# Kernel tuning notes

Hardware: AMD Instinct MI355X
Metric: run time of the kernel (lower is better)

## Reference

```python
import jax, jax.numpy as jnp
import numpy as np

IN_CH, OUT_CH, M1, M2 = 64, 64, 32, 32


def _powerlaw_psd_gaussian(key, exponent, n):
    """JAX port of colorednoise.powerlaw_psd_gaussian (fmin=0 default)."""
    f = jnp.fft.rfftfreq(n).astype(jnp.float32)  # [n//2+1]
    # fmin = max(0, 1/n); f[0]=0 is the only freq below it -> clamp to f[1]
    s_scale = jnp.where(f < 1.0 / n, f[1], f) ** (-exponent / 2.0)
    w = s_scale[1:]
    w = w.at[-1].multiply((1 + (n % 2)) / 2.0)  # Nyquist correction
    sigma = 2.0 * jnp.sqrt(jnp.sum(w * w)) / n
    kr, ki = jax.random.split(key)
    sr = jax.random.normal(kr, f.shape, jnp.float32) * s_scale
    si = jax.random.normal(ki, f.shape, jnp.float32) * s_scale
    if n % 2 == 0:
        si = si.at[-1].set(0.0)
        sr = sr.at[-1].multiply(jnp.sqrt(2.0))
    si = si.at[0].set(0.0)
    sr = sr.at[0].multiply(jnp.sqrt(2.0))
    return jnp.fft.irfft(sr + 1j * si, n=n) / sigma


def _compl_mul2d(t1, w, e_r, e_i, amp_r, amp_i, phi_r, phi_i, key):
    # Faithful to the torch code: stack over in-ch at dim=1 then sum dim=2
    # sums over the OUT channel axis => out[b,i,x,y] = t1[b,i,x,y]*sum_o w[i,o,x,y]
    out = t1 * jnp.sum(w, axis=1)[None]  # [B, IN_CH, M1, M2] complex
    b, c, m1, m2 = out.shape
    n = b * c * m1 * m2
    k1, k2 = jax.random.split(key)
    nr = jnp.roll(_powerlaw_psd_gaussian(k1, e_r, n), phi_r.astype(jnp.int32)) * amp_r
    ni = jnp.roll(_powerlaw_psd_gaussian(k2, e_i, n), phi_i.astype(jnp.int32)) * amp_i
    # original multiplies imag noise by amp_i twice (once in-place, once on reshape)
    noise = (nr + 1j * (ni * amp_i)).reshape(b, c, m1, m2)
    return out - noise


def _forward(x, w1, w2, exp_r, exp_i, nAmp_real, nAmp_imag, nPhase_real, nphase_imag):
    w1c = w1[..., 0] + 1j * w1[..., 1]  # [IN, OUT, M1, M2] complex64
    w2c = w2[..., 0] + 1j * w2[..., 1]
    e_r = jnp.median(exp_r)
    e_i = jnp.median(exp_i)
    amp_r = jnp.median(nAmp_real)
    amp_i = jnp.median(nAmp_imag)
    phi_r = jnp.median(nPhase_real)
    phi_i = jnp.median(nphase_imag)
    B, _, H, W = x.shape
    Wr = W // 2 + 1
    x_ft = jnp.fft.rfft2(x)  # [B, IN_CH, H, Wr]
    key = jax.random.key(42)
    kA, kB = jax.random.split(key)
    out_ft = jnp.zeros((B, OUT_CH, H, Wr), jnp.complex64)
    out_ft = out_ft.at[:, :, :M1, :M2].set(
        _compl_mul2d(x_ft[:, :, :M1, :M2], w1c, e_r, e_i, amp_r, amp_i, phi_r, phi_i, kA))
    out_ft = out_ft.at[:, :, -M1:, :M2].set(
        _compl_mul2d(x_ft[:, :, -M1:, :M2], w2c, e_r, e_i, amp_r, amp_i, phi_r, phi_i, kB))
    return jnp.fft.irfft2(out_ft, s=(H, W)).astype(jnp.float32)


def setup_inputs() -> dict:
    key = jax.random.key(0)
    ks = jax.random.split(key, 9)
    scale = 1.0 / (IN_CH * OUT_CH)
    return {
        "x": jax.random.normal(ks[0], (16, IN_CH, 256, 256), jnp.float32),
        "w1": scale * jax.random.uniform(ks[1], (IN_CH, OUT_CH, M1, M2, 2), jnp.float32),
        "w2": scale * jax.random.uniform(ks[2], (IN_CH, OUT_CH, M1, M2, 2), jnp.float32),
        "exp_r": jax.random.uniform(ks[3], (8,), jnp.float32),
        "exp_i": jax.random.uniform(ks[4], (8,), jnp.float32),
        "nAmp_real": jax.random.uniform(ks[5], (8,), jnp.float32),
        "nAmp_imag": jax.random.uniform(ks[6], (8,), jnp.float32),
        "nPhase_real": jax.random.normal(ks[7], (8,), jnp.float32),
        "nphase_imag": jax.random.normal(ks[8], (8,), jnp.float32),
    }


def reference(x, w1, w2, exp_r, exp_i, nAmp_real, nAmp_imag, nPhase_real, nphase_imag):
    return _forward(x, w1, w2, exp_r, exp_i, nAmp_real, nAmp_imag, nPhase_real, nphase_imag)
```

## Files before the change

kernel.cpp:

```cpp
#include <hip/hip_runtime.h>
#include <cstdint>

#define JPART 1
#define PART_XOR 1

constexpr uint32_t N20   = 1u << 20;
constexpr uint32_t NHALF = 1u << 19;
constexpr int SPT_STRIDE = 520;

struct Hdr {
  float e_r, e_i, amp_r, amp_i;
  int   phi_r, phi_i;
  float nhe_r, nhe_i;
  float scale_s[4];
};
struct KeyArgs { uint32_t k[8][2]; };

typedef __attribute__((ext_vector_type(8))) short short8;
typedef __attribute__((ext_vector_type(16))) float f32x16;

__device__ inline f32x16 zero16() {
  f32x16 v;
  #pragma unroll
  for (int i = 0; i < 16; ++i) v[i] = 0.f;
  return v;
}

__device__ inline unsigned short f2bf(float f) {
  uint32_t u = __float_as_uint(f);
  return (unsigned short)((u + 0x7fffu + ((u >> 16) & 1u)) >> 16);
}

__host__ __device__ inline void tf2x32(uint32_t k0, uint32_t k1, uint32_t x0, uint32_t x1,
                                       uint32_t& o0, uint32_t& o1) {
  const uint32_t ks0 = k0, ks1 = k1, ks2 = k0 ^ k1 ^ 0x1BD11BDAu;
  const uint32_t ks[3] = { ks0, ks1, ks2 };
  x0 += ks0; x1 += ks1;
  const int rot[2][4] = { {13,15,26,6}, {17,29,16,24} };
  for (int g = 0; g < 5; ++g) {
    const int* rr = rot[g & 1];
    for (int i = 0; i < 4; ++i) {
      x0 += x1;
      x1 = (x1 << rr[i]) | (x1 >> (32 - rr[i]));
      x1 ^= x0;
    }
    x0 += ks[(g + 1) % 3];
    x1 += ks[(g + 2) % 3] + (uint32_t)(g + 1);
  }
  o0 = x0; o1 = x1;
}

__device__ inline float erfinv_xla(float x) {
  float w = -log1pf(-x * x);
  float p;
  if (w < 5.0f) {
    w -= 2.5f;
    p = 2.81022636e-08f;
    p = fmaf(p, w, 3.43273939e-07f);
    p = fmaf(p, w, -3.5233877e-06f);
    p = fmaf(p, w, -4.39150654e-06f);
    p = fmaf(p, w, 0.00021858087f);
    p = fmaf(p, w, -0.00125372503f);
    p = fmaf(p, w, -0.00417768164f);
    p = fmaf(p, w, 0.246640727f);
    p = fmaf(p, w, 1.50140941f);
  } else {
    w = sqrtf(w) - 3.0f;
    p = -0.000200214257f;
    p = fmaf(p, w, 0.000100950558f);
    p = fmaf(p, w, 0.00134934322f);
    p = fmaf(p, w, -0.00367342844f);
    p = fmaf(p, w, 0.00573950773f);
    p = fmaf(p, w, -0.0076224613f);
    p = fmaf(p, w, 0.00943887047f);
    p = fmaf(p, w, 1.00167406f);
    p = fmaf(p, w, 2.83297682f);
  }
  return p * x;
}

__device__ inline float normal_from_bits(uint32_t bits) {
  uint32_t fb = (bits >> 9) | 0x3f800000u;
  float f = __uint_as_float(fb) - 1.0f;
  const float LO = -0.99999994f;
  float u = f * 2.0f + LO;
  u = fmaxf(LO, u);
  return 1.41421356f * erfinv_xla(u);
}

__device__ inline float sscale_f(uint32_t k, float nhe) {
  uint32_t kk = k ? k : 1u;
  return powf((float)kk * (1.0f / 1048576.0f), nhe);
}

__device__ inline float2 cmul(float2 a, float2 b) {
  return make_float2(a.x * b.x - a.y * b.y, a.x * b.y + a.y * b.x);
}
__device__ inline float2 wexp(float u) {
  float s, c; sincospif(2.0f * u, &s, &c); return make_float2(c, s);
}
__device__ inline float2 cadd(float2 a, float2 b){ return make_float2(a.x+b.x, a.y+b.y); }
__device__ inline float2 csub(float2 a, float2 b){ return make_float2(a.x-b.x, a.y-b.y); }
__device__ inline float2 cmuli(float2 a){ return make_float2(-a.y, a.x); }

__device__ inline int sA(int p) { return p ^ (((p >> 6) & 3) << 2) ^ ((p >> 8) & 3); }

__device__ inline void bfly(float2& y0, float2& y1, float2& y2, float2& y3, float2 W) {
  float2 a = cadd(y0, y2), b = csub(y0, y2);
  float2 c = cadd(y1, y3), d = cmuli(csub(y1, y3));
  float2 W2 = cmul(W, W), W3 = cmul(W2, W);
  y0 = cadd(a, c);
  y1 = cmul(cadd(b, d), W);
  y2 = cmul(csub(a, c), W2);
  y3 = cmul(csub(b, d), W3);
}

__device__ inline void fft1024_core(float2* r, float2* rc, float2* buf, int w) {
  #pragma unroll
  for (int e3 = 0; e3 < 4; ++e3) {
    float2 W = wexp((float)((e3 << 6) + w) * (1.0f / 1024.0f));
    bfly(r[e3], r[e3 + 4], r[e3 + 8], r[e3 + 12], W);
  }
  {
    float2 W = wexp((float)w * (1.0f / 256.0f));
    #pragma unroll
    for (int e4 = 0; e4 < 4; ++e4)
      bfly(r[(e4 << 2) + 0], r[(e4 << 2) + 1], r[(e4 << 2) + 2], r[(e4 << 2) + 3], W);
  }
  #pragma unroll
  for (int s = 0; s < 16; ++s) buf[sA((s << 6) + w)] = r[s];
  __syncthreads();
  {
    const int e0 = w & 3;
    const int pbase = ((w >> 4) << 8) + (((w >> 2) & 3) << 6) + e0;
    float2 rb[16];
    #pragma unroll
    for (int e2 = 0; e2 < 4; ++e2)
      #pragma unroll
      for (int e1 = 0; e1 < 4; ++e1)
        rb[(e2 << 2) + e1] = buf[sA(pbase + (e2 << 4) + (e1 << 2))];
    #pragma unroll
    for (int e1 = 0; e1 < 4; ++e1) {
      float2 W = wexp((float)((e1 << 2) + e0) * (1.0f / 64.0f));
      bfly(rb[e1], rb[e1 + 4], rb[e1 + 8], rb[e1 + 12], W);
    }
    {
      float2 W = wexp((float)e0 * (1.0f / 16.0f));
      #pragma unroll
      for (int e2 = 0; e2 < 4; ++e2)
        bfly(rb[(e2 << 2) + 0], rb[(e2 << 2) + 1], rb[(e2 << 2) + 2], rb[(e2 << 2) + 3], W);
    }
    #pragma unroll
    for (int e2 = 0; e2 < 4; ++e2)
      #pragma unroll
      for (int e1 = 0; e1 < 4; ++e1)
        buf[sA(pbase + (e2 << 4) + (e1 << 2))] = rb[(e2 << 2) + e1];
  }
  __syncthreads();
  {
    const int cbase = ((w >> 4) << 8) + (((w >> 2) & 3) << 6) + ((w & 3) << 4);
    #pragma unroll
    for (int e1 = 0; e1 < 4; ++e1)
      #pragma unroll
      for (int e0 = 0; e0 < 4; ++e0)
        rc[(e1 << 2) + e0] = buf[sA(cbase + (e1 << 2) + e0)];
    #pragma unroll
    for (int e1 = 0; e1 < 4; ++e1) {
      float2 x0 = rc[(e1 << 2)], x1 = rc[(e1 << 2) + 1], x2 = rc[(e1 << 2) + 2], x3 = rc[(e1 << 2) + 3];
      float2 a = cadd(x0, x2), b = csub(x0, x2);
      float2 c = cadd(x1, x3), d = cmuli(csub(x1, x3));
      rc[(e1 << 2)]     = cadd(a, c);
      rc[(e1 << 2) + 1] = cadd(b, d);
      rc[(e1 << 2) + 2] = csub(a, c);
      rc[(e1 << 2) + 3] = csub(b, d);
    }
  }
}

__device__ inline float med8_dev(const float* p) {
  float v[8];
  for (int i = 0; i < 8; ++i) v[i] = p[i];
  for (int i = 1; i < 8; ++i) { float key = v[i]; int j = i - 1;
    while (j >= 0 && v[j] > key) { v[j + 1] = v[j]; --j; } v[j + 1] = key; }
  return 0.5f * (v[3] + v[4]);
}

__global__ __launch_bounds__(256) void k_misc(Hdr* h,
    const float* er, const float* ei, const float* ar, const float* ai,
    const float* pr, const float* pim,
    const float* __restrict__ w1, const float* __restrict__ w2,
    float2* __restrict__ wsum,
    unsigned short* __restrict__ A_E, unsigned short* __restrict__ B2T,
    unsigned short* __restrict__ ET, unsigned short* __restrict__ Fc,
    unsigned short* __restrict__ Fs, unsigned short* __restrict__ Fns) {
  const int b = blockIdx.x;
  if (b == 960) {
    if (threadIdx.x) return;
    float mer = med8_dev(er), mei = med8_dev(ei);
    h->e_r = mer; h->e_i = mei;
    h->amp_r = med8_dev(ar); h->amp_i = med8_dev(ai);
    h->phi_r = (int)med8_dev(pr);
    h->phi_i = (int)med8_dev(pim);
    h->nhe_r = -0.5f * mer; h->nhe_i = -0.5f * mei;
    return;
  }
  if (b < 512) {
    int idx = b * 256 + threadIdx.x;
    int sel = idx >> 16, rem = idx & 65535;
    const float* w = sel ? w2 : w1;
    int c = rem >> 10, m1 = (rem >> 5) & 31, m2 = rem & 31;
    size_t base = (size_t)c * 131072 + (size_t)m1 * 64 + (size_t)m2 * 2;
    float sr = 0.f, si = 0.f;
    for (int oc = 0; oc < 64; ++oc) { sr += w[base + (size_t)oc * 2048]; si += w[base + (size_t)oc * 2048 + 1]; }
    wsum[idx] = make_float2(sr, si);
    return;
  }
  int t = (b - 512) * 256 + threadIdx.x;
  if (t < 32768) {
    int y = t >> 7, p = t & 127;
    int kyp = p & 63; int ky = (kyp < 32) ? kyp : kyp + 192;
    float s, c; sincospif(2.0f * (float)((ky * y) & 255) * (1.0f / 256.0f), &s, &c);
    A_E[t] = f2bf((p < 64) ? c : s);
  } else if (t < 49152) {
    int u = t - 32768;
    int x = u >> 6, j = u & 63, kx = j & 31;
    float s, c; sincospif(2.0f * (float)((kx * x) & 255) * (1.0f / 256.0f), &s, &c);
    float v = (j < 32) ? ((kx == 0) ? 1.0f : 2.0f * c)
                       : ((kx == 0) ? 0.0f : -2.0f * s);
    B2T[u] = f2bf(v * (1.0f / 65536.0f));
  } else if (t < 65536) {
    int u = t - 49152;
    int col = u >> 8, xx = u & 255; int kx = col & 31;
    float s, c; sincospif(2.0f * (float)((kx * xx) & 255) * (1.0f / 256.0f), &s, &c);
    ET[u] = f2bf((col < 32) ? c : -s);
  } else if (t < 114688) {
    int u = (t - 65536) & 16383;
    int which = (t - 65536) >> 14;
    int kyp = u >> 8, y = u & 255; int ky = (kyp < 32) ? kyp : kyp + 192;
    float s, c; sincospif(2.0f * (float)((ky * y) & 255) * (1.0f / 256.0f), &s, &c);
    if (which == 0) Fc[u] = f2bf(c);
    else if (which == 1) Fs[u] = f2bf(s);
    else Fns[u] = f2bf(-s);
  }
}

__global__ __launch_bounds__(256) void k_gen(const Hdr* __restrict__ h,
                                             float* __restrict__ partials,
                                             float4* __restrict__ spT, KeyArgs ka) {
  __shared__ float sr_[256], si_[256];
  const int b = blockIdx.x;
  if (b < 512) {
    const float nher = h->nhe_r, nhei = h->nhe_i;
    float sr = 0.f, si = 0.f;
    for (int j = 0; j < 4; ++j) {
      uint32_t k = (uint32_t)(b * 1024 + j * 256 + threadIdx.x) + 1u;
      float fk = (float)k * (1.0f / 1048576.0f);
      float wr = powf(fk, nher), wi = powf(fk, nhei);
      if (k == NHALF) { wr *= 0.5f; wi *= 0.5f; }
      sr += wr * wr; si += wi * wi;
    }
    sr_[threadIdx.x] = sr; si_[threadIdx.x] = si; __syncthreads();
    for (int off = 128; off > 0; off >>= 1) {
      if ((int)threadIdx.x < off) { sr_[threadIdx.x] += sr_[threadIdx.x + off];
                                    si_[threadIdx.x] += si_[threadIdx.x + off]; }
      __syncthreads();
    }
    if (!threadIdx.x) { partials[b * 2] = sr_[0]; partials[b * 2 + 1] = si_[0]; }
    return;
  }
  const int idx = b - 512;
  const int pair = idx >> 11;
  const int bx = idx & 2047;
  const int k1 = bx >> 1, chunk = bx & 1;
  const int k2 = (chunk << 8) + (int)threadIdx.x;
  const float nher = h->nhe_r, nhei = h->nhe_i;
  float4* row = spT + (size_t)pair * (1024 * SPT_STRIDE) + (size_t)k1 * SPT_STRIDE;
  const bool extra = (k1 == 0) && (chunk == 1) && (threadIdx.x == 255);
  const int niter = extra ? 2 : 1;
  for (int it = 0; it < niter; ++it) {
    const int kk2 = (it == 0) ? k2 : 512;
    const uint32_t i = (uint32_t)k1 + ((uint32_t)kk2 << 10);
    float vals[4];
    #pragma unroll
    for (int j = 0; j < 4; ++j) {
      const uint32_t K0 = ka.k[pair * 4 + j][0], K1 = ka.k[pair * 4 + j][1];
      uint32_t o0, o1; tf2x32(K0, K1, 0u, i, o0, o1);
#if PART_XOR
      uint32_t bits = o0 ^ o1;
#else
      uint32_t bits = o1;
#endif
      float nhe = (j < 2) ? nher : nhei;
      float v = normal_from_bits(bits) * sscale_f(i, nhe);
      if (i == 0u || i == NHALF) v = (j & 1) ? 0.0f : v * 1.41421356f;
      vals[j] = v;
    }
    row[kk2] = make_float4(vals[0], vals[1], vals[2], vals[3]);
  }
}

__global__ void k_sumw2_fin(Hdr* h, const float* partials) {
  if (threadIdx.x || blockIdx.x) return;
  float Sr = 0.f, Si = 0.f;
  for (int b = 0; b < 512; ++b) { Sr += partials[b * 2]; Si += partials[b * 2 + 1]; }
  float sig_r = 2.0f * sqrtf(Sr) * (1.0f / 1048576.0f);
  float sig_i = 2.0f * sqrtf(Si) * (1.0f / 1048576.0f);
  float s0 = h->amp_r / (sig_r * 1048576.0f);
  float s1 = (h->amp_i * h->amp_i) / (sig_i * 1048576.0f);
  h->scale_s[0] = s0; h->scale_s[1] = s1; h->scale_s[2] = s0; h->scale_s[3] = s1;
}

__global__ __launch_bounds__(256) void k_fft_s1(const float4* __restrict__ spT,
                                                float2* __restrict__ G) {
  __shared__ float2 buf4[4][1024];
  const int b = blockIdx.x;
  const int lin = (b & 7) * 64 + (b >> 3);
  const int pair = lin >> 8;
  const int g = threadIdx.x >> 6, w = threadIdx.x & 63;
  const int k1b = (lin & 255) << 2;
  const int k1 = k1b + g;
  const float4* sp = spT + (size_t)pair * (1024 * SPT_STRIDE);
  const int mrow = (1024 - k1) & 1023;

  float2 r[16], rc[16];
  #pragma unroll
  for (int s = 0; s < 16; ++s) {
    int k2 = (s << 6) + w;
    uint32_t k = (uint32_t)k1 + ((uint32_t)k2 << 10);
    float4 f; float2 z;
    if (k <= NHALF) {
      f = sp[(size_t)k1 * SPT_STRIDE + k2];
      z = make_float2(f.x - f.w, f.y + f.z);
    } else {
      int k2p = (k1 == 0) ? (1024 - k2) : (1023 - k2);
      f = sp[(size_t)mrow * SPT_STRIDE + k2p];
      z = make_float2(f.x + f.w, f.z - f.y);
    }
    r[s] = z;
  }
  fft1024_core(r, rc, buf4[g], w);
  const int klo = ((w & 3) << 4) + (((w >> 2) & 3) << 2) + (w >> 4);
  #pragma unroll
  for (int e1 = 0; e1 < 4; ++e1)
    #pragma unroll
    for (int e0 = 0; e0 < 4; ++e0) {
      int k = (e0 << 8) + (e1 << 6) + klo;
      float2 tw = wexp((float)(k * k1) * (1.0f / 1048576.0f));
      buf4[g][sA(k)] = cmul(rc[(e1 << 2) + e0], tw);
    }
  __syncthreads();
  const int t = threadIdx.x;
  float2* gp = G + ((size_t)pair << 20) + (size_t)k1b;
  const int k1off = t & 3;
  #pragma unroll
  for (int it = 0; it < 16; ++it) {
    int j2 = (it << 6) + (t >> 2);
    gp[((size_t)j2 << 10) + k1off] = buf4[k1off][sA(j2)];
  }
}

__global__ __launch_bounds__(256) void k_fft_s2(const float2* __restrict__ G,
                                                float2* __restrict__ noiseP,
                                                const Hdr* __restrict__ h) {
  __shared__ float2 buf4[4][1024];
  const int b = blockIdx.x;
  const int lin = (b & 7) * 64 + (b >> 3);
  const int pair = lin >> 8;
  const int g = threadIdx.x >> 6, w = threadIdx.x & 63;
  const int j2 = ((lin & 255) << 2) + g;

  float2 r[16], rc[16];
  const float2* gp = G + ((size_t)pair << 20) + ((size_t)j2 << 10);
  #pragma unroll
  for (int s = 0; s < 16; ++s) r[s] = gp[(s << 6) + w];
  fft1024_core(r, rc, buf4[g], w);
  const float scr = h->scale_s[0], sci = h->scale_s[1];
  float2* np_ = noiseP + ((size_t)pair << 20) + ((size_t)j2 << 10);
  const int klo = ((w & 3) << 4) + (((w >> 2) & 3) << 2) + (w >> 4);
  #pragma unroll
  for (int e1 = 0; e1 < 4; ++e1)
    #pragma unroll
    for (int e0 = 0; e0 < 4; ++e0) {
      int k = (e0 << 8) + (e1 << 6) + klo;
      np_[k] = make_float2(rc[(e1 << 2) + e0].x * scr, rc[(e1 << 2) + e0].y * sci);
    }
}

__global__ __launch_bounds__(256) void k_ntrans(const float2* __restrict__ noiseP,
                                                float* __restrict__ noiseL,
                                                const Hdr* __restrict__ h) {
  __shared__ float tr[64][65];
  __shared__ float ti[64][65];
  const int b = blockIdx.x;
  const int pair = b >> 8, tid = b & 255;
  const int R0 = (tid >> 4) << 6;
  const int C0 = (tid & 15) << 6;
  const int t = threadIdx.x;
  const int tx = t & 63, ty = t >> 6;
  const int phir = h->phi_r, phii = h->phi_i;
  const float2* src = noiseP + ((size_t)pair << 20);
  float* dstr = noiseL + ((size_t)(pair * 2) << 20);
  float* dsti = noiseL + ((size_t)(pair * 2 + 1) << 20);
  #pragma unroll
  for (int i = 0; i < 16; ++i) {
    int r = (i << 2) + ty;
    float2 v = src[(size_t)((R0 + r) << 10) + (size_t)(C0 + tx)];
    tr[r][tx] = v.x; ti[r][tx] = v.y;
  }
  __syncthreads();
  #pragma unroll
  for (int i = 0; i < 16; ++i) {
    int c = (i << 2) + ty;
    int n = ((C0 + c) << 10) + R0 + tx;
    dstr[(uint32_t)(n + phir) & (N20 - 1u)] = tr[tx][c];
    dsti[(uint32_t)(n + phii) & (N20 - 1u)] = ti[tx][c];
  }
}

__global__ __launch_bounds__(256, 2) void k_forward(const float* __restrict__ x,
    const float2* __restrict__ wsum, const float* __restrict__ noiseL,
    const unsigned short* __restrict__ ET, const unsigned short* __restrict__ Fc,
    const unsigned short* __restrict__ Fs, const unsigned short* __restrict__ Fns,
    float2* __restrict__ oftg) {
  __shared__ char lds[65536];
  char* X1T = lds + 32768;
  const int bc = blockIdx.x, t = threadIdx.x;
  const int c = bc & 63;
  const int l = t & 63, w = t >> 6, lr = l & 31, kg = l >> 5;
  const int rt = w >> 1, ct = w & 1;
  const float* xim = x + ((size_t)bc << 16);

  float4 pf[16];
  #pragma unroll
  for (int i = 0; i < 16; ++i) {
    int f4 = i * 256 + t;
    int r = f4 >> 6, c4 = f4 & 63;
    pf[i] = *(const float4*)(xim + (size_t)((r) << 8) + (c4 << 2));
  }

  #pragma unroll
  for (int yt = 0; yt < 4; ++yt) {
    __syncthreads();
    #pragma unroll
    for (int i = 0; i < 16; ++i) {
      int f4 = i * 256 + t;
      int r = f4 >> 6, c4 = f4 & 63;
      ushort4 b4; b4.x = f2bf(pf[i].x); b4.y = f2bf(pf[i].y);
      b4.z = f2bf(pf[i].z); b4.w = f2bf(pf[i].w);
      int byte = ((r << 9) + (c4 << 3)) ^ ((r & 7) << 4);
      *(ushort4*)(lds + byte) = b4;
    }
    __syncthreads();
    if (yt < 3) {
      #pragma unroll
      for (int i = 0; i < 16; ++i) {
        int f4 = i * 256 + t;
        int r = f4 >> 6, c4 = f4 & 63;
        pf[i] = *(const float4*)(xim + (size_t)((((yt + 1) << 6) + r) << 8) + (c4 << 2));
      }
    }
    f32x16 a1 = zero16();
    const int arow = (rt << 5) + lr;
    const int bcol = (ct << 5) + lr;
    #pragma unroll
    for (int s = 0; s < 16; ++s) {
      short8 af = *(const short8*)(lds + (((arow << 9) + (s << 5) + (kg << 4)) ^ ((arow & 7) << 4)));
      short8 bf = *(const short8*)(ET + (bcol << 8) + (s << 4) + (kg << 3));
      a1 = __builtin_amdgcn_mfma_f32_32x32x16_bf16(af, bf, a1, 0, 0, 0);
    }
    #pragma unroll
    for (int r4 = 0; r4 < 4; ++r4) {
      int y0 = (yt << 6) + (rt << 5) + (r4 << 3) + (kg << 2);
      ushort4 p4;
      p4.x = f2bf(a1[r4 * 4 + 0]); p4.y = f2bf(a1[r4 * 4 + 1]);
      p4.z = f2bf(a1[r4 * 4 + 2]); p4.w = f2bf(a1[r4 * 4 + 3]);
      int byte = ((bcol << 9) + (y0 << 1)) ^ ((bcol & 7) << 4);
      *(ushort4*)(X1T + byte) = p4;
    }
  }
  __syncthreads();

  const int re_im = w >> 1, kt = w & 1;
  const unsigned short* A1p = re_im ? Fns : Fs;
  const int b0row = (re_im ? 32 : 0) + lr;
  const int b1row = (re_im ? 0 : 32) + lr;
  const int a2row = (kt << 5) + lr;
  f32x16 a2 = zero16();
  #pragma unroll
  for (int s = 0; s < 16; ++s) {
    short8 a0f = *(const short8*)(Fc  + (a2row << 8) + (s << 4) + (kg << 3));
    short8 a1f = *(const short8*)(A1p + (a2row << 8) + (s << 4) + (kg << 3));
    short8 b0f = *(const short8*)(X1T + (((b0row << 9) + (s << 5) + (kg << 4)) ^ ((b0row & 7) << 4)));
    short8 b1f = *(const short8*)(X1T + (((b1row << 9) + (s << 5) + (kg << 4)) ^ ((b1row & 7) << 4)));
    a2 = __builtin_amdgcn_mfma_f32_32x32x16_bf16(a0f, b0f, a2, 0, 0, 0);
    a2 = __builtin_amdgcn_mfma_f32_32x32x16_bf16(a1f, b1f, a2, 0, 0, 0);
  }
  float* Osm = (float*)(lds + (re_im << 13));
  #pragma unroll
  for (int i = 0; i < 16; ++i) {
    int row = (kt << 5) + (i & 3) + ((i >> 2) << 3) + (kg << 2);
    Osm[(row << 5) + lr] = a2[i];
  }
  __syncthreads();

  const float* Ore = (const float*)lds;
  const float* Oim = (const float*)(lds + 8192);
  #pragma unroll
  for (int r = 0; r < 8; ++r) {
    int idx = (r << 8) + t;
    int kyp = idx >> 5, kx = idx & 31;
    int sel = kyp >> 5, m1 = kyp & 31;
    float2 av = make_float2(Ore[idx], Oim[idx]);
    float2 wv = wsum[((size_t)sel << 16) + (size_t)(((c << 5) | m1) << 5) + (size_t)kx];
    float2 v;
    v.x = av.x * wv.x - av.y * wv.y;
    v.y = av.x * wv.y + av.y * wv.x;
    uint32_t p = ((uint32_t)((bc << 5) | m1) << 5) | (uint32_t)kx;
    const float* nlr = noiseL + ((size_t)(sel ? 2 : 0) << 20);
    const float* nli = noiseL + ((size_t)(sel ? 3 : 1) << 20);
    v.x -= nlr[p];
    v.y -= nli[p];
    oftg[((size_t)bc << 11) + (size_t)idx] = v;
  }
}

__global__ __launch_bounds__(256) void k_inverse(const float2* __restrict__ oftg,
    const unsigned short* __restrict__ A_E, const unsigned short* __restrict__ B2T,
    float* __restrict__ out) {
  __shared__ char smem[32768];

  const int bc = blockIdx.x, t = threadIdx.x;
  const int l = t & 63, w = t >> 6, lr = l & 31, kg = l >> 5;

  {
    const float* ob = (const float*)(oftg + ((size_t)bc << 11));
    #pragma unroll
    for (int i = 0; i < 32; ++i) {
      int idx = t + (i << 8);
      int p = idx >> 6, j = idx & 63;
      int kyp = p & 63;
      float v;
      if (p < 64) v = (j < 32) ? ob[(kyp << 6) + (j << 1)]
                               : ob[(kyp << 6) + ((j - 32) << 1) + 1];
      else        v = (j < 32) ? -ob[(kyp << 6) + (j << 1) + 1]
                               : ob[(kyp << 6) + ((j - 32) << 1)];
      int byte = ((j << 8) + (p << 1)) ^ ((j & 7) << 4);
      *(unsigned short*)(smem + byte) = f2bf(v);
    }
  }
  __syncthreads();

  f32x16 acc[2][2];
  acc[0][0] = zero16(); acc[0][1] = zero16(); acc[1][0] = zero16(); acc[1][1] = zero16();
  #pragma unroll
  for (int s = 0; s < 8; ++s) {
    short8 af[2], bf[2];
    #pragma unroll
    for (int rt = 0; rt < 2; ++rt) {
      int row = (w << 6) + (rt << 5) + lr;
      af[rt] = *(const short8*)(A_E + (row << 7) + (s << 4) + (kg << 3));
    }
    #pragma unroll
    for (int ct = 0; ct < 2; ++ct) {
      int j = (ct << 5) + lr;
      int byte = ((j << 8) + (s << 5) + (kg << 4)) ^ ((j & 7) << 4);
      bf[ct] = *(const short8*)(smem + byte);
    }
    #pragma unroll
    for (int rt = 0; rt < 2; ++rt)
      #pragma unroll
      for (int ct = 0; ct < 2; ++ct)
        acc[rt][ct] = __builtin_amdgcn_mfma_f32_32x32x16_bf16(af[rt], bf[ct], acc[rt][ct], 0, 0, 0);
  }
  __syncthreads();

  #pragma unroll
  for (int rt = 0; rt < 2; ++rt)
    #pragma unroll
    for (int ct = 0; ct < 2; ++ct)
      #pragma unroll
      for (int r = 0; r < 16; ++r) {
        int row = (w << 6) + (rt << 5) + (r & 3) + (((r >> 2) & 3) << 3) + (kg << 2);
        int col = (ct << 5) + lr;
        int byte = ((row << 7) + (col << 1)) ^ ((row & 7) << 4);
        *(unsigned short*)(smem + byte) = f2bf(acc[rt][ct][r]);
      }
  __syncthreads();

  short8 ta[2][4];
  #pragma unroll
  for (int rt = 0; rt < 2; ++rt)
    #pragma unroll
    for (int ks = 0; ks < 4; ++ks) {
      int row = (w << 6) + (rt << 5) + lr;
      int byte = ((row << 7) + (ks << 5) + (kg << 4)) ^ ((row & 7) << 4);
      ta[rt][ks] = *(const short8*)(smem + byte);
    }
  float* op = out + ((size_t)bc << 16);
  #pragma unroll
  for (int cc = 0; cc < 4; ++cc) {
    short8 b2[2][4];
    #pragma unroll
    for (int cx = 0; cx < 2; ++cx)
      #pragma unroll
      for (int ks = 0; ks < 4; ++ks) {
        int xx = (cc << 6) + (cx << 5) + lr;
        b2[cx][ks] = *(const short8*)(B2T + (xx << 6) + (ks << 4) + (kg << 3));
      }
    f32x16 a2[2][2];
    a2[0][0] = zero16(); a2[0][1] = zero16(); a2[1][0] = zero16(); a2[1][1] = zero16();
    #pragma unroll
    for (int ks = 0; ks < 4; ++ks)
      #pragma unroll
      for (int rt = 0; rt < 2; ++rt)
        #pragma unroll
        for (int cx = 0; cx < 2; ++cx)
          a2[rt][cx] = __builtin_amdgcn_mfma_f32_32x32x16_bf16(ta[rt][ks], b2[cx][ks], a2[rt][cx], 0, 0, 0);
    #pragma unroll
    for (int rt = 0; rt < 2; ++rt)
      #pragma unroll
      for (int cx = 0; cx < 2; ++cx)
        #pragma unroll
        for (int r = 0; r < 16; ++r) {
          int row = (w << 6) + (rt << 5) + (r & 3) + (((r >> 2) & 3) << 3) + (kg << 2);
          int xx = (cc << 6) + (cx << 5) + lr;
          op[(row << 8) + xx] = a2[rt][cx][r];
        }
  }
}

extern "C" void kernel_launch(void* const* d_in, const int* in_sizes, int n_in,
                              void* d_out, int out_size, void* d_ws, size_t ws_size,
                              hipStream_t stream) {
  (void)in_sizes; (void)n_in; (void)out_size; (void)ws_size;
  const float* x   = (const float*)d_in[0];
  const float* w1  = (const float*)d_in[1];
  const float* w2  = (const float*)d_in[2];
  const float* er  = (const float*)d_in[3];
  const float* ei  = (const float*)d_in[4];
  const float* ar  = (const float*)d_in[5];
  const float* ai  = (const float*)d_in[6];
  const float* pr  = (const float*)d_in[7];
  const float* pim = (const float*)d_in[8];
  float* out = (float*)d_out;

  char* ws = (char*)d_ws;
  Hdr*    hdr      = (Hdr*)ws;
  float*  partials = (float*)(ws + 0x1000);
  float2* wsum     = (float2*)(ws + 0x10000);
  unsigned short* A_E = (unsigned short*)(ws + 0x130000);
  unsigned short* B2T = (unsigned short*)(ws + 0x140000);
  unsigned short* ET  = (unsigned short*)(ws + 0x148000);
  unsigned short* Fc  = (unsigned short*)(ws + 0x150000);
  unsigned short* Fs  = (unsigned short*)(ws + 0x158000);
  unsigned short* Fns = (unsigned short*)(ws + 0x160000);
  float4* spT      = (float4*)(ws + 0x200000);
  float2* G        = (float2*)(ws + 0x1400000);
  float2* oft      = (float2*)(ws + 0x1400000);
  float2* noiseP   = (float2*)(ws + 0x2400000);
  float*  noiseL   = (float*)(ws + 0x3400000);

  auto splitk = [](const uint32_t k[2], uint32_t a[2], uint32_t b[2]) {
#if JPART
    tf2x32(k[0], k[1], 0u, 0u, a[0], a[1]);
    tf2x32(k[0], k[1], 0u, 1u, b[0], b[1]);
#else
    uint32_t r0[2], r1[2];
    tf2x32(k[0], k[1], 0u, 2u, r0[0], r0[1]);
    tf2x32(k[0], k[1], 1u, 3u, r1[0], r1[1]);
    a[0] = r0[0]; a[1] = r1[0]; b[0] = r0[1]; b[1] = r1[1];
#endif
  };
  uint32_t root[2] = { 0u, 42u };
  uint32_t kA[2], kB[2], k1A[2], k2A[2], k1B[2], k2B[2];
  splitk(root, kA, kB);
  splitk(kA, k1A, k2A);
  splitk(kB, k1B, k2B);
  KeyArgs ka;
  splitk(k1A, ka.k[0], ka.k[1]);
  splitk(k2A, ka.k[2], ka.k[3]);
  splitk(k1B, ka.k[4], ka.k[5]);
  splitk(k2B, ka.k[6], ka.k[7]);

  hipLaunchKernelGGL(k_misc,      dim3(961),      dim3(256), 0, stream, hdr, er, ei, ar, ai, pr, pim,
                     w1, w2, wsum, A_E, B2T, ET, Fc, Fs, Fns);
  hipLaunchKernelGGL(k_gen,       dim3(4608),     dim3(256), 0, stream, hdr, partials, spT, ka);
  hipLaunchKernelGGL(k_sumw2_fin, dim3(1),        dim3(64),  0, stream, hdr, partials);
  hipLaunchKernelGGL(k_fft_s1,    dim3(512),      dim3(256), 0, stream, spT, G);
  hipLaunchKernelGGL(k_fft_s2,    dim3(512),      dim3(256), 0, stream, G, noiseP, hdr);
  hipLaunchKernelGGL(k_ntrans,    dim3(512),      dim3(256), 0, stream, noiseP, noiseL, hdr);
  hipLaunchKernelGGL(k_forward,   dim3(1024),     dim3(256), 0, stream, x, wsum, noiseL, ET, Fc, Fs, Fns, oft);
  hipLaunchKernelGGL(k_inverse,   dim3(1024),     dim3(256), 0, stream, oft, A_E, B2T, out);
}
```

Measured before the change: 264.0 us.

## Merge noise generation with forward DFT and move noise subtraction into inverse

The noise-spectrum generation blocks and the forward DFT blocks now run in a single launch, since the forward transform no longer depends on the noise. The noise subtraction moves from the forward kernel into the inverse kernel's staging loop. The sigma finalisation is folded into the first FFT stage as an extra block. Together this removes two launches and lets the independent forward work overlap the noise pipeline. In exchange, the combined kernel needs 64KB of LDS for every block, including the light gen blocks, which may reduce their occupancy, and noiseL now shares workspace with spT.

```diff
diff --git a/kernel.cpp b/kernel.cpp
--- a/kernel.cpp
+++ b/kernel.cpp
@@ -244,12 +244,17 @@
   }
 }
 
-__global__ __launch_bounds__(256) void k_gen(const Hdr* __restrict__ h,
-                                             float* __restrict__ partials,
-                                             float4* __restrict__ spT, KeyArgs ka) {
-  __shared__ float sr_[256], si_[256];
+__global__ __launch_bounds__(256, 2) void k_gen_fwd(const Hdr* __restrict__ h,
+    float* __restrict__ partials, float4* __restrict__ spT, KeyArgs ka,
+    const float* __restrict__ x, const float2* __restrict__ wsum,
+    const unsigned short* __restrict__ ET, const unsigned short* __restrict__ Fc,
+    const unsigned short* __restrict__ Fs, const unsigned short* __restrict__ Fns,
+    float2* __restrict__ oftg) {
+  __shared__ char lds[65536];
   const int b = blockIdx.x;
   if (b < 512) {
+    float* sr_ = (float*)lds;
+    float* si_ = (float*)(lds + 1024);
     const float nher = h->nhe_r, nhei = h->nhe_i;
     float sr = 0.f, si = 0.f;
     for (int j = 0; j < 4; ++j) {
@@ -268,52 +273,151 @@
     if (!threadIdx.x) { partials[b * 2] = sr_[0]; partials[b * 2 + 1] = si_[0]; }
     return;
   }
-  const int idx = b - 512;
-  const int pair = idx >> 11;
-  const int bx = idx & 2047;
-  const int k1 = bx >> 1, chunk = bx & 1;
-  const int k2 = (chunk << 8) + (int)threadIdx.x;
-  const float nher = h->nhe_r, nhei = h->nhe_i;
-  float4* row = spT + (size_t)pair * (1024 * SPT_STRIDE) + (size_t)k1 * SPT_STRIDE;
-  const bool extra = (k1 == 0) && (chunk == 1) && (threadIdx.x == 255);
-  const int niter = extra ? 2 : 1;
-  for (int it = 0; it < niter; ++it) {
-    const int kk2 = (it == 0) ? k2 : 512;
-    const uint32_t i = (uint32_t)k1 + ((uint32_t)kk2 << 10);
-    float vals[4];
-    #pragma unroll
-    for (int j = 0; j < 4; ++j) {
-      const uint32_t K0 = ka.k[pair * 4 + j][0], K1 = ka.k[pair * 4 + j][1];
-      uint32_t o0, o1; tf2x32(K0, K1, 0u, i, o0, o1);
+  if (b < 4608) {
+    const int idx = b - 512;
+    const int pair = idx >> 11;
+    const int bx = idx & 2047;
+    const int k1 = bx >> 1, chunk = bx & 1;
+    const int k2 = (chunk << 8) + (int)threadIdx.x;
+    const float nher = h->nhe_r, nhei = h->nhe_i;
+    float4* row = spT + (size_t)pair * (1024 * SPT_STRIDE) + (size_t)k1 * SPT_STRIDE;
+    const bool extra = (k1 == 0) && (chunk == 1) && (threadIdx.x == 255);
+    const int niter = extra ? 2 : 1;
+    for (int it = 0; it < niter; ++it) {
+      const int kk2 = (it == 0) ? k2 : 512;
+      const uint32_t i = (uint32_t)k1 + ((uint32_t)kk2 << 10);
+      float vals[4];
+      #pragma unroll
+      for (int j = 0; j < 4; ++j) {
+        const uint32_t K0 = ka.k[pair * 4 + j][0], K1 = ka.k[pair * 4 + j][1];
+        uint32_t o0, o1; tf2x32(K0, K1, 0u, i, o0, o1);
 #if PART_XOR
-      uint32_t bits = o0 ^ o1;
+        uint32_t bits = o0 ^ o1;
 #else
-      uint32_t bits = o1;
+        uint32_t bits = o1;
 #endif
-      float nhe = (j < 2) ? nher : nhei;
-      float v = normal_from_bits(bits) * sscale_f(i, nhe);
-      if (i == 0u || i == NHALF) v = (j & 1) ? 0.0f : v * 1.41421356f;
-      vals[j] = v;
-    }
-    row[kk2] = make_float4(vals[0], vals[1], vals[2], vals[3]);
-  }
-}
-
-__global__ void k_sumw2_fin(Hdr* h, const float* partials) {
-  if (threadIdx.x || blockIdx.x) return;
-  float Sr = 0.f, Si = 0.f;
-  for (int b = 0; b < 512; ++b) { Sr += partials[b * 2]; Si += partials[b * 2 + 1]; }
-  float sig_r = 2.0f * sqrtf(Sr) * (1.0f / 1048576.0f);
-  float sig_i = 2.0f * sqrtf(Si) * (1.0f / 1048576.0f);
-  float s0 = h->amp_r / (sig_r * 1048576.0f);
-  float s1 = (h->amp_i * h->amp_i) / (sig_i * 1048576.0f);
-  h->scale_s[0] = s0; h->scale_s[1] = s1; h->scale_s[2] = s0; h->scale_s[3] = s1;
-}
-
-__global__ __launch_bounds__(256) void k_fft_s1(const float4* __restrict__ spT,
+        float nhe = (j < 2) ? nher : nhei;
+        float v = normal_from_bits(bits) * sscale_f(i, nhe);
+        if (i == 0u || i == NHALF) v = (j & 1) ? 0.0f : v * 1.41421356f;
+        vals[j] = v;
+      }
+      row[kk2] = make_float4(vals[0], vals[1], vals[2], vals[3]);
+    }
+    return;
+  }
+
+  char* X1T = lds + 32768;
+  const int bc = b - 4608, t = threadIdx.x;
+  const int c = bc & 63;
+  const int l = t & 63, w = t >> 6, lr = l & 31, kg = l >> 5;
+  const int rt = w >> 1, ct = w & 1;
+  const float* xim = x + ((size_t)bc << 16);
+
+  float4 pf[16];
+  #pragma unroll
+  for (int i = 0; i < 16; ++i) {
+    int f4 = i * 256 + t;
+    int r = f4 >> 6, c4 = f4 & 63;
+    pf[i] = *(const float4*)(xim + (size_t)((r) << 8) + (c4 << 2));
+  }
+
+  #pragma unroll
+  for (int yt = 0; yt < 4; ++yt) {
+    __syncthreads();
+    #pragma unroll
+    for (int i = 0; i < 16; ++i) {
+      int f4 = i * 256 + t;
+      int r = f4 >> 6, c4 = f4 & 63;
+      ushort4 b4; b4.x = f2bf(pf[i].x); b4.y = f2bf(pf[i].y);
+      b4.z = f2bf(pf[i].z); b4.w = f2bf(pf[i].w);
+      int byte = ((r << 9) + (c4 << 3)) ^ ((r & 7) << 4);
+      *(ushort4*)(lds + byte) = b4;
+    }
+    __syncthreads();
+    if (yt < 3) {
+      #pragma unroll
+      for (int i = 0; i < 16; ++i) {
+        int f4 = i * 256 + t;
+        int r = f4 >> 6, c4 = f4 & 63;
+        pf[i] = *(const float4*)(xim + (size_t)((((yt + 1) << 6) + r) << 8) + (c4 << 2));
+      }
+    }
+    f32x16 a1 = zero16();
+    const int arow = (rt << 5) + lr;
+    const int bcol = (ct << 5) + lr;
+    #pragma unroll
+    for (int s = 0; s < 16; ++s) {
+      short8 af = *(const short8*)(lds + (((arow << 9) + (s << 5) + (kg << 4)) ^ ((arow & 7) << 4)));
+      short8 bf = *(const short8*)(ET + (bcol << 8) + (s << 4) + (kg << 3));
+      a1 = __builtin_amdgcn_mfma_f32_32x32x16_bf16(af, bf, a1, 0, 0, 0);
+    }
+    #pragma unroll
+    for (int r4 = 0; r4 < 4; ++r4) {
+      int y0 = (yt << 6) + (rt << 5) + (r4 << 3) + (kg << 2);
+      ushort4 p4;
+      p4.x = f2bf(a1[r4 * 4 + 0]); p4.y = f2bf(a1[r4 * 4 + 1]);
+      p4.z = f2bf(a1[r4 * 4 + 2]); p4.w = f2bf(a1[r4 * 4 + 3]);
+      int byte = ((bcol << 9) + (y0 << 1)) ^ ((bcol & 7) << 4);
+      *(ushort4*)(X1T + byte) = p4;
+    }
+  }
+  __syncthreads();
+
+  const int re_im = w >> 1, kt = w & 1;
+  const unsigned short* A1p = re_im ? Fns : Fs;
+  const int b0row = (re_im ? 32 : 0) + lr;
+  const int b1row = (re_im ? 0 : 32) + lr;
+  const int a2row = (kt << 5) + lr;
+  f32x16 a2 = zero16();
+  #pragma unroll
+  for (int s = 0; s < 16; ++s) {
+    short8 a0f = *(const short8*)(Fc  + (a2row << 8) + (s << 4) + (kg << 3));
+    short8 a1f = *(const short8*)(A1p + (a2row << 8) + (s << 4) + (kg << 3));
+    short8 b0f = *(const short8*)(X1T + (((b0row << 9) + (s << 5) + (kg << 4)) ^ ((b0row & 7) << 4)));
+    short8 b1f = *(const short8*)(X1T + (((b1row << 9) + (s << 5) + (kg << 4)) ^ ((b1row & 7) << 4)));
+    a2 = __builtin_amdgcn_mfma_f32_32x32x16_bf16(a0f, b0f, a2, 0, 0, 0);
+    a2 = __builtin_amdgcn_mfma_f32_32x32x16_bf16(a1f, b1f, a2, 0, 0, 0);
+  }
+  float* Osm = (float*)(lds + (re_im << 13));
+  #pragma unroll
+  for (int i = 0; i < 16; ++i) {
+    int row = (kt << 5) + (i & 3) + ((i >> 2) << 3) + (kg << 2);
+    Osm[(row << 5) + lr] = a2[i];
+  }
+  __syncthreads();
+
+  const float* Ore = (const float*)lds;
+  const float* Oim = (const float*)(lds + 8192);
+  #pragma unroll
+  for (int r = 0; r < 8; ++r) {
+    int idx = (r << 8) + t;
+    int kyp = idx >> 5, kx = idx & 31;
+    int sel = kyp >> 5, m1 = kyp & 31;
+    float2 av = make_float2(Ore[idx], Oim[idx]);
+    float2 wv = wsum[((size_t)sel << 16) + (size_t)(((c << 5) | m1) << 5) + (size_t)kx];
+    float2 v;
+    v.x = av.x * wv.x - av.y * wv.y;
+    v.y = av.x * wv.y + av.y * wv.x;
+    oftg[((size_t)bc << 11) + (size_t)idx] = v;
+  }
+}
+
+__global__ __launch_bounds__(256) void k_fin_s1(Hdr* h, const float* __restrict__ partials,
+                                                const float4* __restrict__ spT,
                                                 float2* __restrict__ G) {
   __shared__ float2 buf4[4][1024];
   const int b = blockIdx.x;
+  if (b == 512) {
+    if (threadIdx.x) return;
+    float Sr = 0.f, Si = 0.f;
+    for (int q = 0; q < 512; ++q) { Sr += partials[q * 2]; Si += partials[q * 2 + 1]; }
+    float sig_r = 2.0f * sqrtf(Sr) * (1.0f / 1048576.0f);
+    float sig_i = 2.0f * sqrtf(Si) * (1.0f / 1048576.0f);
+    float s0 = h->amp_r / (sig_r * 1048576.0f);
+    float s1 = (h->amp_i * h->amp_i) / (sig_i * 1048576.0f);
+    h->scale_s[0] = s0; h->scale_s[1] = s1; h->scale_s[2] = s0; h->scale_s[3] = s1;
+    return;
+  }
   const int lin = (b & 7) * 64 + (b >> 3);
   const int pair = lin >> 8;
   const int g = threadIdx.x >> 6, w = threadIdx.x & 63;
@@ -417,114 +521,8 @@
   }
 }
 
-__global__ __launch_bounds__(256, 2) void k_forward(const float* __restrict__ x,
-    const float2* __restrict__ wsum, const float* __restrict__ noiseL,
-    const unsigned short* __restrict__ ET, const unsigned short* __restrict__ Fc,
-    const unsigned short* __restrict__ Fs, const unsigned short* __restrict__ Fns,
-    float2* __restrict__ oftg) {
-  __shared__ char lds[65536];
-  char* X1T = lds + 32768;
-  const int bc = blockIdx.x, t = threadIdx.x;
-  const int c = bc & 63;
-  const int l = t & 63, w = t >> 6, lr = l & 31, kg = l >> 5;
-  const int rt = w >> 1, ct = w & 1;
-  const float* xim = x + ((size_t)bc << 16);
-
-  float4 pf[16];
-  #pragma unroll
-  for (int i = 0; i < 16; ++i) {
-    int f4 = i * 256 + t;
-    int r = f4 >> 6, c4 = f4 & 63;
-    pf[i] = *(const float4*)(xim + (size_t)((r) << 8) + (c4 << 2));
-  }
-
-  #pragma unroll
-  for (int yt = 0; yt < 4; ++yt) {
-    __syncthreads();
-    #pragma unroll
-    for (int i = 0; i < 16; ++i) {
-      int f4 = i * 256 + t;
-      int r = f4 >> 6, c4 = f4 & 63;
-      ushort4 b4; b4.x = f2bf(pf[i].x); b4.y = f2bf(pf[i].y);
-      b4.z = f2bf(pf[i].z); b4.w = f2bf(pf[i].w);
-      int byte = ((r << 9) + (c4 << 3)) ^ ((r & 7) << 4);
-      *(ushort4*)(lds + byte) = b4;
-    }
-    __syncthreads();
-    if (yt < 3) {
-      #pragma unroll
-      for (int i = 0; i < 16; ++i) {
-        int f4 = i * 256 + t;
-        int r = f4 >> 6, c4 = f4 & 63;
-        pf[i] = *(const float4*)(xim + (size_t)((((yt + 1) << 6) + r) << 8) + (c4 << 2));
-      }
-    }
-    f32x16 a1 = zero16();
-    const int arow = (rt << 5) + lr;
-    const int bcol = (ct << 5) + lr;
-    #pragma unroll
-    for (int s = 0; s < 16; ++s) {
-      short8 af = *(const short8*)(lds + (((arow << 9) + (s << 5) + (kg << 4)) ^ ((arow & 7) << 4)));
-      short8 bf = *(const short8*)(ET + (bcol << 8) + (s << 4) + (kg << 3));
-      a1 = __builtin_amdgcn_mfma_f32_32x32x16_bf16(af, bf, a1, 0, 0, 0);
-    }
-    #pragma unroll
-    for (int r4 = 0; r4 < 4; ++r4) {
-      int y0 = (yt << 6) + (rt << 5) + (r4 << 3) + (kg << 2);
-      ushort4 p4;
-      p4.x = f2bf(a1[r4 * 4 + 0]); p4.y = f2bf(a1[r4 * 4 + 1]);
-      p4.z = f2bf(a1[r4 * 4 + 2]); p4.w = f2bf(a1[r4 * 4 + 3]);
-      int byte = ((bcol << 9) + (y0 << 1)) ^ ((bcol & 7) << 4);
-      *(ushort4*)(X1T + byte) = p4;
-    }
-  }
-  __syncthreads();
-
-  const int re_im = w >> 1, kt = w & 1;
-  const unsigned short* A1p = re_im ? Fns : Fs;
-  const int b0row = (re_im ? 32 : 0) + lr;
-  const int b1row = (re_im ? 0 : 32) + lr;
-  const int a2row = (kt << 5) + lr;
-  f32x16 a2 = zero16();
-  #pragma unroll
-  for (int s = 0; s < 16; ++s) {
-    short8 a0f = *(const short8*)(Fc  + (a2row << 8) + (s << 4) + (kg << 3));
-    short8 a1f = *(const short8*)(A1p + (a2row << 8) + (s << 4) + (kg << 3));
-    short8 b0f = *(const short8*)(X1T + (((b0row << 9) + (s << 5) + (kg << 4)) ^ ((b0row & 7) << 4)));
-    short8 b1f = *(const short8*)(X1T + (((b1row << 9) + (s << 5) + (kg << 4)) ^ ((b1row & 7) << 4)));
-    a2 = __builtin_amdgcn_mfma_f32_32x32x16_bf16(a0f, b0f, a2, 0, 0, 0);
-    a2 = __builtin_amdgcn_mfma_f32_32x32x16_bf16(a1f, b1f, a2, 0, 0, 0);
-  }
-  float* Osm = (float*)(lds + (re_im << 13));
-  #pragma unroll
-  for (int i = 0; i < 16; ++i) {
-    int row = (kt << 5) + (i & 3) + ((i >> 2) << 3) + (kg << 2);
-    Osm[(row << 5) + lr] = a2[i];
-  }
-  __syncthreads();
-
-  const float* Ore = (const float*)lds;
-  const float* Oim = (const float*)(lds + 8192);
-  #pragma unroll
-  for (int r = 0; r < 8; ++r) {
-    int idx = (r << 8) + t;
-    int kyp = idx >> 5, kx = idx & 31;
-    int sel = kyp >> 5, m1 = kyp & 31;
-    float2 av = make_float2(Ore[idx], Oim[idx]);
-    float2 wv = wsum[((size_t)sel << 16) + (size_t)(((c << 5) | m1) << 5) + (size_t)kx];
-    float2 v;
-    v.x = av.x * wv.x - av.y * wv.y;
-    v.y = av.x * wv.y + av.y * wv.x;
-    uint32_t p = ((uint32_t)((bc << 5) | m1) << 5) | (uint32_t)kx;
-    const float* nlr = noiseL + ((size_t)(sel ? 2 : 0) << 20);
-    const float* nli = noiseL + ((size_t)(sel ? 3 : 1) << 20);
-    v.x -= nlr[p];
-    v.y -= nli[p];
-    oftg[((size_t)bc << 11) + (size_t)idx] = v;
-  }
-}
-
 __global__ __launch_bounds__(256) void k_inverse(const float2* __restrict__ oftg,
+    const float* __restrict__ noiseL,
     const unsigned short* __restrict__ A_E, const unsigned short* __restrict__ B2T,
     float* __restrict__ out) {
   __shared__ char smem[32768];
@@ -534,16 +532,22 @@
 
   {
     const float* ob = (const float*)(oftg + ((size_t)bc << 11));
+    const uint32_t pbase = (uint32_t)bc << 10;
     #pragma unroll
     for (int i = 0; i < 32; ++i) {
       int idx = t + (i << 8);
       int p = idx >> 6, j = idx & 63;
       int kyp = p & 63;
+      int sel = kyp >> 5, m1 = kyp & 31;
+      const float* nlr = noiseL + ((size_t)(sel ? 2 : 0) << 20);
+      const float* nli = noiseL + ((size_t)(sel ? 3 : 1) << 20);
+      int kx = (j < 32) ? j : (j - 32);
+      uint32_t pn = pbase + ((uint32_t)m1 << 5) + (uint32_t)kx;
       float v;
-      if (p < 64) v = (j < 32) ? ob[(kyp << 6) + (j << 1)]
-                               : ob[(kyp << 6) + ((j - 32) << 1) + 1];
-      else        v = (j < 32) ? -ob[(kyp << 6) + (j << 1) + 1]
-                               : ob[(kyp << 6) + ((j - 32) << 1)];
+      if (p < 64) v = (j < 32) ? (ob[(kyp << 6) + (j << 1)] - nlr[pn])
+                               : (ob[(kyp << 6) + ((j - 32) << 1) + 1] - nli[pn]);
+      else        v = (j < 32) ? -(ob[(kyp << 6) + (j << 1) + 1] - nli[pn])
+                               : (ob[(kyp << 6) + ((j - 32) << 1)] - nlr[pn]);
       int byte = ((j << 8) + (p << 1)) ^ ((j & 7) << 4);
       *(unsigned short*)(smem + byte) = f2bf(v);
     }
@@ -655,10 +659,10 @@
   unsigned short* Fs  = (unsigned short*)(ws + 0x158000);
   unsigned short* Fns = (unsigned short*)(ws + 0x160000);
   float4* spT      = (float4*)(ws + 0x200000);
+  float*  noiseL   = (float*)(ws + 0x200000);
   float2* G        = (float2*)(ws + 0x1400000);
-  float2* oft      = (float2*)(ws + 0x1400000);
   float2* noiseP   = (float2*)(ws + 0x2400000);
-  float*  noiseL   = (float*)(ws + 0x3400000);
+  float2* oft      = (float2*)(ws + 0x3400000);
 
   auto splitk = [](const uint32_t k[2], uint32_t a[2], uint32_t b[2]) {
 #if JPART
@@ -682,13 +686,12 @@
   splitk(k1B, ka.k[4], ka.k[5]);
   splitk(k2B, ka.k[6], ka.k[7]);
 
-  hipLaunchKernelGGL(k_misc,      dim3(961),      dim3(256), 0, stream, hdr, er, ei, ar, ai, pr, pim,
+  hipLaunchKernelGGL(k_misc,    dim3(961),  dim3(256), 0, stream, hdr, er, ei, ar, ai, pr, pim,
                      w1, w2, wsum, A_E, B2T, ET, Fc, Fs, Fns);
-  hipLaunchKernelGGL(k_gen,       dim3(4608),     dim3(256), 0, stream, hdr, partials, spT, ka);
-  hipLaunchKernelGGL(k_sumw2_fin, dim3(1),        dim3(64),  0, stream, hdr, partials);
-  hipLaunchKernelGGL(k_fft_s1,    dim3(512),      dim3(256), 0, stream, spT, G);
-  hipLaunchKernelGGL(k_fft_s2,    dim3(512),      dim3(256), 0, stream, G, noiseP, hdr);
-  hipLaunchKernelGGL(k_ntrans,    dim3(512),      dim3(256), 0, stream, noiseP, noiseL, hdr);
-  hipLaunchKernelGGL(k_forward,   dim3(1024),     dim3(256), 0, stream, x, wsum, noiseL, ET, Fc, Fs, Fns, oft);
-  hipLaunchKernelGGL(k_inverse,   dim3(1024),     dim3(256), 0, stream, oft, A_E, B2T, out);
-}
+  hipLaunchKernelGGL(k_gen_fwd, dim3(5632), dim3(256), 0, stream, hdr, partials, spT, ka,
+                     x, wsum, ET, Fc, Fs, Fns, oft);
+  hipLaunchKernelGGL(k_fin_s1,  dim3(513),  dim3(256), 0, stream, hdr, partials, spT, G);
+  hipLaunchKernelGGL(k_fft_s2,  dim3(512),  dim3(256), 0, stream, G, noiseP, hdr);
+  hipLaunchKernelGGL(k_ntrans,  dim3(512),  dim3(256), 0, stream, noiseP, noiseL, hdr);
+  hipLaunchKernelGGL(k_inverse, dim3(1024), dim3(256), 0, stream, oft, noiseL, A_E, B2T, out);
+}
```

New measurement: 260.5 us, median of 2. No clear change (-1.3%).
